# Performance work log

Measured on AMD Instinct MI355X. Metric: run time of the kernel, lower is better.

## Reference

```python
import jax, jax.numpy as jnp
import numpy as np

L, K, H = 8192, 30, 128
SCALE = 30.0
LN_EPS = 1e-5


def _ln(x, g, b):
    mu = jnp.mean(x, axis=-1, keepdims=True)
    var = jnp.mean((x - mu) ** 2, axis=-1, keepdims=True)
    return (x - mu) * jax.lax.rsqrt(var + LN_EPS) * g + b


def _gelu(x):
    return jax.nn.gelu(x, approximate=False)  # torch.nn.GELU default (exact)


def setup_inputs() -> dict:
    key = jax.random.key(0)
    ks = jax.random.split(key, 16)

    def lin(k, din, dout):
        k1, k2 = jax.random.split(k)
        w = jax.random.normal(k1, (din, dout), jnp.float32) / np.sqrt(din).astype(np.float32)
        b = jax.random.normal(k2, (dout,), jnp.float32) * 0.01
        return w, b

    inp = {}
    inp['h_V'] = jax.random.normal(ks[0], (L, H), jnp.float32)
    inp['h_E'] = jax.random.normal(ks[1], (L, K, H), jnp.float32)
    inp['E_idx'] = jax.random.randint(ks[2], (L, K), 0, L, jnp.int32)
    inp['mask_V'] = jnp.ones((L,), jnp.float32)
    inp['mask_attend'] = jnp.ones((L, K), jnp.float32)

    D_in = 3 * H  # num_hidden + num_in = 128 + 256
    inp['W1'], inp['b1'] = lin(ks[3], D_in, H)
    inp['W2'], inp['b2'] = lin(ks[4], H, H)
    inp['W3'], inp['b3'] = lin(ks[5], H, H)
    inp['W11'], inp['b11'] = lin(ks[6], D_in, H)
    inp['W12'], inp['b12'] = lin(ks[7], H, H)
    inp['W13'], inp['b13'] = lin(ks[8], H, H)
    inp['Wi'], inp['bi'] = lin(ks[9], H, 4 * H)   # PositionWiseFeedForward.W_in
    inp['Wo'], inp['bo'] = lin(ks[10], 4 * H, H)  # PositionWiseFeedForward.W_out
    inp['g1'] = jnp.ones((H,), jnp.float32); inp['be1'] = jnp.zeros((H,), jnp.float32)
    inp['g2'] = jnp.ones((H,), jnp.float32); inp['be2'] = jnp.zeros((H,), jnp.float32)
    inp['g3'] = jnp.ones((H,), jnp.float32); inp['be3'] = jnp.zeros((H,), jnp.float32)
    return inp


def _forward(h_V, h_E, E_idx, mask_V, mask_attend,
             W1, b1, W2, b2, W3, b3, W11, b11, W12, b12, W13, b13,
             Wi, bi, Wo, bo, g1, be1, g2, be2, g3, be3):
    # --- node update: gather neighbors, concat, 3-layer MLP message, masked sum ---
    h_nb = h_V[E_idx]                                   # [L,K,H] gather_nodes
    h_EV = jnp.concatenate(
        [jnp.broadcast_to(h_V[:, None, :], (L, K, H)), h_E, h_nb], axis=-1)  # [L,K,3H]
    m = _gelu(h_EV @ W1 + b1)
    m = _gelu(m @ W2 + b2)
    m = m @ W3 + b3                                     # [L,K,H]
    m = mask_attend[..., None] * m
    dh = jnp.sum(m, axis=-2) / SCALE                    # [L,H]
    h_V = _ln(h_V + dh, g1, be1)
    # --- position-wise FFN ---
    dh = _gelu(h_V @ Wi + bi) @ Wo + bo
    h_V = _ln(h_V + dh, g2, be2)
    h_V = mask_V[:, None] * h_V
    # --- edge update ---
    h_nb = h_V[E_idx]
    h_EV = jnp.concatenate(
        [jnp.broadcast_to(h_V[:, None, :], (L, K, H)), h_E, h_nb], axis=-1)
    m = _gelu(h_EV @ W11 + b11)
    m = _gelu(m @ W12 + b12)
    m = m @ W13 + b13
    h_E = _ln(h_E + m, g3, be3)
    return h_V, h_E


def reference(h_V, h_E, E_idx, mask_V, mask_attend,
              W1, b1, W2, b2, W3, b3, W11, b11, W12, b12, W13, b13,
              Wi, bi, Wo, bo, g1, be1, g2, be2, g3, be3):
    return _forward(h_V, h_E, E_idx, mask_V, mask_attend,
                    W1, b1, W2, b2, W3, b3, W11, b11, W12, b12, W13, b13,
                    Wi, bi, Wo, bo, g1, be1, g2, be2, g3, be3)
```

## Files before the change

kernel.cpp:

```cpp
#include <hip/hip_runtime.h>
#include <math.h>

typedef unsigned short u16;
typedef __bf16 bf16x8 __attribute__((ext_vector_type(8)));
typedef float f32x4 __attribute__((ext_vector_type(4)));
typedef u16 u16x8 __attribute__((ext_vector_type(8)));

#define LTOT 8192
#define KNB  30
#define HDIM 128

__device__ __forceinline__ float bf2f(u16 u){
  unsigned x = ((unsigned)u) << 16;
  return __builtin_bit_cast(float, x);
}
__device__ __forceinline__ u16 f2bf(float f){
  unsigned x = __builtin_bit_cast(unsigned, f);
  x = x + 0x7fffu + ((x >> 16) & 1u);
  return (u16)(x >> 16);
}
__device__ __forceinline__ float gelu_f(float x){
  float u = 0.7978845608028654f * (x + 0.044715f * x * x * x);
  float e = __expf(2.f * u);
  float t = 1.f - 2.f / (e + 1.f);
  return 0.5f * x * (1.f + t);
}
__device__ __forceinline__ void pack8(u16* dst, const float* s){
  float4 a = *(const float4*)s, b = *(const float4*)(s + 4);
  u16x8 p;
  p[0]=f2bf(a.x); p[1]=f2bf(a.y); p[2]=f2bf(a.z); p[3]=f2bf(a.w);
  p[4]=f2bf(b.x); p[5]=f2bf(b.y); p[6]=f2bf(b.z); p[7]=f2bf(b.w);
  *(u16x8*)dst = p;
}

struct TEnt { const float* src; u16* dst; int K; int N; int nb; };
struct TTab { TEnt e[12]; };

__global__ __launch_bounds__(256) void transpose_kernel(TTab t){
  int b = (int)blockIdx.x;
  for (int i = 0; i < 12; ++i){
    int nb = t.e[i].nb;
    if (b < nb){
      int N = t.e[i].N, Kd = t.e[i].K;
      int idx = b * 256 + (int)threadIdx.x;
      if (idx < Kd * N){
        int k = idx / N;
        int n = idx - k * N;
        t.e[i].dst[n * Kd + k] = f2bf(t.e[i].src[(long)k * N + n]);
      }
      return;
    }
    b -= nb;
  }
}

template<bool XF32>
__global__ __launch_bounds__(256) void pre_gemm_kernel(
  const void* __restrict__ X,
  const u16* __restrict__ WTa, const float* __restrict__ ba, u16* __restrict__ outa,
  const u16* __restrict__ WTc, u16* __restrict__ outc)
{
  __shared__ __align__(16) char smem[8704];
  u16* Xs = (u16*)smem;
  const int tid = threadIdx.x;
  const int wave = tid >> 6, lane = tid & 63, q = lane >> 4, s = lane & 15;
  const int row0 = (int)blockIdx.x * 32;

  for (int i = tid; i < 32 * 16; i += 256){
    int r = i >> 4, cb = i & 15;
    if (XF32) pack8(&Xs[r * 136 + cb * 8], &((const float*)X)[(long)(row0 + r) * HDIM + cb * 8]);
    else *(u16x8*)&Xs[r * 136 + cb * 8] = *(const u16x8*)&((const u16*)X)[(long)(row0 + r) * HDIM + cb * 8];
  }
  __syncthreads();
  for (int w = 0; w < 2; ++w){
    const u16* W = w ? WTc : WTa;
    u16* out = w ? outc : outa;
    f32x4 acc[2][2];
#pragma unroll
    for (int mt = 0; mt < 2; ++mt)
#pragma unroll
      for (int nt = 0; nt < 2; ++nt){ f32x4 z = {0.f,0.f,0.f,0.f}; acc[mt][nt] = z; }
    for (int kt = 0; kt < 4; ++kt){
      bf16x8 b0 = *(const bf16x8*)&W[(wave * 32 + s) * 128 + kt * 32 + q * 8];
      bf16x8 b1 = *(const bf16x8*)&W[(wave * 32 + 16 + s) * 128 + kt * 32 + q * 8];
#pragma unroll
      for (int mt = 0; mt < 2; ++mt){
        bf16x8 af = *(const bf16x8*)&Xs[(mt * 16 + s) * 136 + kt * 32 + q * 8];
        acc[mt][0] = __builtin_amdgcn_mfma_f32_16x16x32_bf16(af, b0, acc[mt][0], 0, 0, 0);
        acc[mt][1] = __builtin_amdgcn_mfma_f32_16x16x32_bf16(af, b1, acc[mt][1], 0, 0, 0);
      }
    }
#pragma unroll
    for (int nt = 0; nt < 2; ++nt){
      int col = wave * 32 + nt * 16 + s;
      float bv = w ? 0.f : ba[col];
#pragma unroll
      for (int mt = 0; mt < 2; ++mt)
#pragma unroll
        for (int r = 0; r < 4; ++r){
          int row = row0 + mt * 16 + q * 4 + r;
          out[(long)row * HDIM + col] = f2bf(acc[mt][nt][r] + bv);
        }
    }
  }
}

template<bool EDGE>
__global__ __launch_bounds__(256, 4) void msg_kernel(
  const float* __restrict__ hVin,
  const float* __restrict__ hE,
  const int* __restrict__ Eidx,
  const float* __restrict__ maskA,
  const u16* __restrict__ vsum,
  const u16* __restrict__ vcg,
  const u16* __restrict__ WTb, const u16* __restrict__ WT2, const u16* __restrict__ WT3,
  const float* __restrict__ b2, const float* __restrict__ b3,
  const float* __restrict__ gam, const float* __restrict__ bet,
  float* __restrict__ out_f32,
  u16* __restrict__ out_b16,
  float* __restrict__ outE)
{
  __shared__ __align__(16) char smem[18944];
  u16*   As   = (u16*)smem;
  float* ovl  = (float*)smem;
  float* vbuf = (float*)(smem + 17408);
  float* mbuf = (float*)(smem + 18432);
  int*   nbr  = (int*)(smem + 18688);

  const int tid = threadIdx.x;
  const int wave = tid >> 6, lane = tid & 63, q = lane >> 4, s = lane & 15;
  const int node0 = (int)blockIdx.x * 2;

  for (int i = tid; i < 64 * 16; i += 256){
    int r = i >> 4, cb = i & 15, nd = r >> 5, k = r & 31;
    if (k < KNB)
      pack8(&As[r * 136 + cb * 8], &hE[(((long)(node0 + nd) * KNB) + k) * HDIM + cb * 8]);
    else { u16x8 z = {0,0,0,0,0,0,0,0}; *(u16x8*)&As[r * 136 + cb * 8] = z; }
  }
  if (tid < 64){
    int nd = tid >> 5, k = tid & 31;
    int e = (node0 + nd) * KNB + k;
    bool v = (k < KNB);
    nbr[tid] = v ? Eidx[e] : 0;
    if (!EDGE) mbuf[tid] = v ? maskA[e] : 0.f;
  }
  vbuf[tid] = bf2f(vsum[(long)(node0 + (tid >> 7)) * HDIM + (tid & 127)]);

  f32x4 acc[4][2];
  for (int layer = 0; layer < 3; ++layer){
    const u16* W = (layer == 0) ? WTb : ((layer == 1) ? WT2 : WT3);
    __syncthreads();
#pragma unroll
    for (int mt = 0; mt < 4; ++mt){ f32x4 z = {0.f,0.f,0.f,0.f}; acc[mt][0] = z; acc[mt][1] = z; }
    for (int kt = 0; kt < 4; ++kt){
      bf16x8 b0 = *(const bf16x8*)&W[(wave * 32 + s) * 128 + kt * 32 + q * 8];
      bf16x8 b1 = *(const bf16x8*)&W[(wave * 32 + 16 + s) * 128 + kt * 32 + q * 8];
#pragma unroll
      for (int mt = 0; mt < 4; ++mt){
        bf16x8 af = *(const bf16x8*)&As[(mt * 16 + s) * 136 + kt * 32 + q * 8];
        acc[mt][0] = __builtin_amdgcn_mfma_f32_16x16x32_bf16(af, b0, acc[mt][0], 0, 0, 0);
        acc[mt][1] = __builtin_amdgcn_mfma_f32_16x16x32_bf16(af, b1, acc[mt][1], 0, 0, 0);
      }
    }
    if (layer < 2){
      __syncthreads();
#pragma unroll
      for (int nt = 0; nt < 2; ++nt){
        int col = wave * 32 + nt * 16 + s;
        float bv = (layer == 1) ? b2[col] : 0.f;
#pragma unroll
        for (int mt = 0; mt < 4; ++mt)
#pragma unroll
          for (int r = 0; r < 4; ++r){
            int row = mt * 16 + q * 4 + r;
            float v = acc[mt][nt][r] + bv;
            if (layer == 0)
              v += vbuf[((row >> 5) << 7) + col] + bf2f(vcg[(long)nbr[row] * HDIM + col]);
            As[row * 136 + col] = f2bf(gelu_f(v));
          }
      }
    }
  }
  __syncthreads();

  if (!EDGE){
    float* dh = ovl;
#pragma unroll
    for (int nt = 0; nt < 2; ++nt){
      int col = wave * 32 + nt * 16 + s;
      float b3v = b3[col];
#pragma unroll
      for (int ni = 0; ni < 2; ++ni){
        float ss = 0.f;
#pragma unroll
        for (int mh = 0; mh < 2; ++mh){
          int mt = ni * 2 + mh;
#pragma unroll
          for (int r = 0; r < 4; ++r){
            int row = mt * 16 + q * 4 + r;
            ss += (acc[mt][nt][r] + b3v) * mbuf[row];
          }
        }
        ss += __shfl_xor(ss, 16);
        ss += __shfl_xor(ss, 32);
        if (q == 0) dh[ni * 128 + col] = ss * (1.f / 30.f);
      }
    }
    __syncthreads();
    if (wave < 2){
      int node = node0 + wave;
      float x0 = hVin[(long)node * HDIM + lane]      + dh[wave * 128 + lane];
      float x1 = hVin[(long)node * HDIM + 64 + lane] + dh[wave * 128 + 64 + lane];
      float sm = x0 + x1, s2 = x0 * x0 + x1 * x1;
#pragma unroll
      for (int o = 32; o; o >>= 1){ sm += __shfl_xor(sm, o); s2 += __shfl_xor(s2, o); }
      float mu = sm * (1.f / 128.f);
      float var = fmaxf(s2 * (1.f / 128.f) - mu * mu, 0.f);
      float rs = rsqrtf(var + 1e-5f);
      float y0 = (x0 - mu) * rs * gam[lane]      + bet[lane];
      float y1 = (x1 - mu) * rs * gam[64 + lane] + bet[64 + lane];
      out_f32[(long)node * HDIM + lane]      = y0;
      out_f32[(long)node * HDIM + 64 + lane] = y1;
      out_b16[(long)node * HDIM + lane]      = f2bf(y0);
      out_b16[(long)node * HDIM + 64 + lane] = f2bf(y1);
    }
  } else {
    float* part  = ovl;
    float* part2 = ovl + 256;
    float* muv   = ovl + 512;
    float* rsv   = ovl + 576;
#pragma unroll
    for (int nt = 0; nt < 2; ++nt){
      int col = wave * 32 + nt * 16 + s;
      float b3v = b3[col];
#pragma unroll
      for (int mt = 0; mt < 4; ++mt)
#pragma unroll
        for (int r = 0; r < 4; ++r){
          int row = mt * 16 + q * 4 + r, nd = row >> 5, k = row & 31;
          float z = acc[mt][nt][r] + b3v;
          if (k < KNB) z += hE[(((long)(node0 + nd) * KNB) + k) * HDIM + col];
          acc[mt][nt][r] = z;
        }
    }
#pragma unroll
    for (int mt = 0; mt < 4; ++mt)
#pragma unroll
      for (int r = 0; r < 4; ++r){
        int row = mt * 16 + q * 4 + r;
        float ps = acc[mt][0][r] + acc[mt][1][r];
        float pq = acc[mt][0][r] * acc[mt][0][r] + acc[mt][1][r] * acc[mt][1][r];
#pragma unroll
        for (int o = 1; o < 16; o <<= 1){ ps += __shfl_xor(ps, o); pq += __shfl_xor(pq, o); }
        if (s == 0){ part[row * 4 + wave] = ps; part2[row * 4 + wave] = pq; }
      }
    __syncthreads();
    if (tid < 64){
      float sm = part[tid*4] + part[tid*4+1] + part[tid*4+2] + part[tid*4+3];
      float sq = part2[tid*4] + part2[tid*4+1] + part2[tid*4+2] + part2[tid*4+3];
      float mu = sm * (1.f / 128.f);
      float var = fmaxf(sq * (1.f / 128.f) - mu * mu, 0.f);
      muv[tid] = mu;
      rsv[tid] = rsqrtf(var + 1e-5f);
    }
    __syncthreads();
#pragma unroll
    for (int nt = 0; nt < 2; ++nt){
      int col = wave * 32 + nt * 16 + s;
      float gv = gam[col], bv = bet[col];
#pragma unroll
      for (int mt = 0; mt < 4; ++mt)
#pragma unroll
        for (int r = 0; r < 4; ++r){
          int row = mt * 16 + q * 4 + r, nd = row >> 5, k = row & 31;
          if (k < KNB){
            float y = (acc[mt][nt][r] - muv[row]) * rsv[row] * gv + bv;
            outE[(((long)(node0 + nd) * KNB) + k) * HDIM + col] = y;
          }
        }
    }
  }
}

__global__ __launch_bounds__(256) void ffn_kernel(
  const u16* __restrict__ xb, const float* __restrict__ xf,
  const u16* __restrict__ WiT,
  const u16* __restrict__ WoT,
  const float* __restrict__ bi, const float* __restrict__ bo,
  const float* __restrict__ g2, const float* __restrict__ be2,
  const float* __restrict__ maskV,
  float* __restrict__ outV, u16* __restrict__ hv2)
{
  __shared__ __align__(16) char smem[18816];
  u16*   Xs = (u16*)smem;
  u16*   Ts = (u16*)(smem + 8704);
  float* part  = (float*)(smem + 17408);
  float* part2 = part + 128;
  float* muv   = part + 256;
  float* rsv   = part + 288;
  const int tid = threadIdx.x;
  const int wave = tid >> 6, lane = tid & 63, q = lane >> 4, s = lane & 15;
  const int row0 = (int)blockIdx.x * 32;

  for (int i = tid; i < 32 * 16; i += 256){
    int r = i >> 4, cb = i & 15;
    *(u16x8*)&Xs[r * 136 + cb * 8] = *(const u16x8*)&xb[(long)(row0 + r) * HDIM + cb * 8];
  }
  f32x4 yac[2][2];
#pragma unroll
  for (int mt = 0; mt < 2; ++mt)
#pragma unroll
    for (int nt = 0; nt < 2; ++nt){ f32x4 z = {0.f,0.f,0.f,0.f}; yac[mt][nt] = z; }

  for (int j = 0; j < 4; ++j){
    __syncthreads();
    f32x4 tac[2][2];
#pragma unroll
    for (int mt = 0; mt < 2; ++mt)
#pragma unroll
      for (int nt = 0; nt < 2; ++nt){ f32x4 z = {0.f,0.f,0.f,0.f}; tac[mt][nt] = z; }
    for (int kt = 0; kt < 4; ++kt){
      bf16x8 b0 = *(const bf16x8*)&WiT[((long)(j * 128 + wave * 32 + s)) * 128 + kt * 32 + q * 8];
      bf16x8 b1 = *(const bf16x8*)&WiT[((long)(j * 128 + wave * 32 + 16 + s)) * 128 + kt * 32 + q * 8];
#pragma unroll
      for (int mt = 0; mt < 2; ++mt){
        bf16x8 af = *(const bf16x8*)&Xs[(mt * 16 + s) * 136 + kt * 32 + q * 8];
        tac[mt][0] = __builtin_amdgcn_mfma_f32_16x16x32_bf16(af, b0, tac[mt][0], 0, 0, 0);
        tac[mt][1] = __builtin_amdgcn_mfma_f32_16x16x32_bf16(af, b1, tac[mt][1], 0, 0, 0);
      }
    }
#pragma unroll
    for (int nt = 0; nt < 2; ++nt){
      int col = wave * 32 + nt * 16 + s;
      float bv = bi[j * 128 + col];
#pragma unroll
      for (int mt = 0; mt < 2; ++mt)
#pragma unroll
        for (int r = 0; r < 4; ++r){
          int row = mt * 16 + q * 4 + r;
          Ts[row * 136 + col] = f2bf(gelu_f(tac[mt][nt][r] + bv));
        }
    }
    __syncthreads();
    for (int kt = 0; kt < 4; ++kt){
      bf16x8 b0 = *(const bf16x8*)&WoT[((long)(wave * 32 + s)) * 512 + j * 128 + kt * 32 + q * 8];
      bf16x8 b1 = *(const bf16x8*)&WoT[((long)(wave * 32 + 16 + s)) * 512 + j * 128 + kt * 32 + q * 8];
#pragma unroll
      for (int mt = 0; mt < 2; ++mt){
        bf16x8 af = *(const bf16x8*)&Ts[(mt * 16 + s) * 136 + kt * 32 + q * 8];
        yac[mt][0] = __builtin_amdgcn_mfma_f32_16x16x32_bf16(af, b0, yac[mt][0], 0, 0, 0);
        yac[mt][1] = __builtin_amdgcn_mfma_f32_16x16x32_bf16(af, b1, yac[mt][1], 0, 0, 0);
      }
    }
  }
#pragma unroll
  for (int nt = 0; nt < 2; ++nt){
    int col = wave * 32 + nt * 16 + s;
    float bv = bo[col];
#pragma unroll
    for (int mt = 0; mt < 2; ++mt)
#pragma unroll
      for (int r = 0; r < 4; ++r){
        int row = mt * 16 + q * 4 + r;
        yac[mt][nt][r] += bv + xf[(long)(row0 + row) * HDIM + col];
      }
  }
#pragma unroll
  for (int mt = 0; mt < 2; ++mt)
#pragma unroll
    for (int r = 0; r < 4; ++r){
      int row = mt * 16 + q * 4 + r;
      float ps = yac[mt][0][r] + yac[mt][1][r];
      float pq = yac[mt][0][r] * yac[mt][0][r] + yac[mt][1][r] * yac[mt][1][r];
#pragma unroll
      for (int o = 1; o < 16; o <<= 1){ ps += __shfl_xor(ps, o); pq += __shfl_xor(pq, o); }
      if (s == 0){ part[row * 4 + wave] = ps; part2[row * 4 + wave] = pq; }
    }
  __syncthreads();
  if (tid < 32){
    float sm = part[tid*4] + part[tid*4+1] + part[tid*4+2] + part[tid*4+3];
    float sq = part2[tid*4] + part2[tid*4+1] + part2[tid*4+2] + part2[tid*4+3];
    float mu = sm * (1.f / 128.f);
    float var = fmaxf(sq * (1.f / 128.f) - mu * mu, 0.f);
    muv[tid] = mu;
    rsv[tid] = rsqrtf(var + 1e-5f);
  }
  __syncthreads();
#pragma unroll
  for (int nt = 0; nt < 2; ++nt){
    int col = wave * 32 + nt * 16 + s;
    float gv = g2[col], bv = be2[col];
#pragma unroll
    for (int mt = 0; mt < 2; ++mt)
#pragma unroll
      for (int r = 0; r < 4; ++r){
        int row = mt * 16 + q * 4 + r;
        float y = (yac[mt][nt][r] - muv[row]) * rsv[row] * gv + bv;
        y *= maskV[row0 + row];
        outV[(long)(row0 + row) * HDIM + col] = y;
        hv2[(long)(row0 + row) * HDIM + col] = f2bf(y);
      }
  }
}

extern "C" void kernel_launch(void* const* d_in, const int* in_sizes, int n_in,
                              void* d_out, int out_size, void* d_ws, size_t ws_size,
                              hipStream_t stream) {
  const float* hV    = (const float*)d_in[0];
  const float* hE    = (const float*)d_in[1];
  const int*   Eidx  = (const int*)d_in[2];
  const float* maskV = (const float*)d_in[3];
  const float* maskA = (const float*)d_in[4];
  const float* W1  = (const float*)d_in[5];  const float* b1  = (const float*)d_in[6];
  const float* W2  = (const float*)d_in[7];  const float* b2  = (const float*)d_in[8];
  const float* W3  = (const float*)d_in[9];  const float* b3  = (const float*)d_in[10];
  const float* W11 = (const float*)d_in[11]; const float* b11 = (const float*)d_in[12];
  const float* W12 = (const float*)d_in[13]; const float* b12 = (const float*)d_in[14];
  const float* W13 = (const float*)d_in[15]; const float* b13 = (const float*)d_in[16];
  const float* Wi  = (const float*)d_in[17]; const float* bi  = (const float*)d_in[18];
  const float* Wo  = (const float*)d_in[19]; const float* bo  = (const float*)d_in[20];
  const float* g1  = (const float*)d_in[21]; const float* be1 = (const float*)d_in[22];
  const float* g2  = (const float*)d_in[23]; const float* be2 = (const float*)d_in[24];
  const float* g3  = (const float*)d_in[25]; const float* be3 = (const float*)d_in[26];

  char* ws = (char*)d_ws;
  u16* wt = (u16*)ws;
  u16* wtW1a  = wt;
  u16* wtW1b  = wt + 16384;
  u16* wtW1c  = wt + 32768;
  u16* wtW2   = wt + 49152;
  u16* wtW3   = wt + 65536;
  u16* wtW11a = wt + 81920;
  u16* wtW11b = wt + 98304;
  u16* wtW11c = wt + 114688;
  u16* wtW12  = wt + 131072;
  u16* wtW13  = wt + 147456;
  u16* wtWi   = wt + 163840;
  u16* wtWo   = wt + 229376;
  size_t off = 589824;
  u16* vsum1   = (u16*)(ws + off); off += 2097152;
  u16* vc      = (u16*)(ws + off); off += 2097152;
  u16* vsum11  = (u16*)(ws + off); off += 2097152;
  u16* vc2     = (u16*)(ws + off); off += 2097152;
  float* hv1_f32 = (float*)(ws + off); off += 4194304;
  u16*   hv1_b16 = (u16*)(ws + off);   off += 2097152;
  u16*   hv2_b16 = (u16*)(ws + off);   off += 2097152;

  float* outV = (float*)d_out;
  float* outE = (float*)d_out + (long)LTOT * HDIM;

  TTab tt;
  tt.e[0]  = { W1,          wtW1a,  128, 128, 64 };
  tt.e[1]  = { W1 + 16384,  wtW1b,  128, 128, 64 };
  tt.e[2]  = { W1 + 32768,  wtW1c,  128, 128, 64 };
  tt.e[3]  = { W2,          wtW2,   128, 128, 64 };
  tt.e[4]  = { W3,          wtW3,   128, 128, 64 };
  tt.e[5]  = { W11,         wtW11a, 128, 128, 64 };
  tt.e[6]  = { W11 + 16384, wtW11b, 128, 128, 64 };
  tt.e[7]  = { W11 + 32768, wtW11c, 128, 128, 64 };
  tt.e[8]  = { W12,         wtW12,  128, 128, 64 };
  tt.e[9]  = { W13,         wtW13,  128, 128, 64 };
  tt.e[10] = { Wi,          wtWi,   128, 512, 256 };
  tt.e[11] = { Wo,          wtWo,   512, 128, 256 };
  transpose_kernel<<<dim3(1152), dim3(256), 0, stream>>>(tt);

  pre_gemm_kernel<true><<<dim3(256), dim3(256), 0, stream>>>(
      hV, wtW1a, b1, vsum1, wtW1c, vc);
  msg_kernel<false><<<dim3(4096), dim3(256), 0, stream>>>(
      hV, hE, Eidx, maskA, vsum1, vc, wtW1b, wtW2, wtW3, b2, b3, g1, be1,
      hv1_f32, hv1_b16, nullptr);
  ffn_kernel<<<dim3(256), dim3(256), 0, stream>>>(
      hv1_b16, hv1_f32, wtWi, wtWo, bi, bo, g2, be2, maskV, outV, hv2_b16);
  pre_gemm_kernel<false><<<dim3(256), dim3(256), 0, stream>>>(
      hv2_b16, wtW11a, b11, vsum11, wtW11c, vc2);
  msg_kernel<true><<<dim3(4096), dim3(256), 0, stream>>>(
      hV, hE, Eidx, maskA, vsum11, vc2, wtW11b, wtW12, wtW13, b12, b13, g3, be3,
      hv1_f32, hv1_b16, outE);
}
```

Before: 463.2 us.

## Stage gathered neighbor rows in LDS and cheapen GELU and bf16 conversion

The kernel now copies the gathered neighbor rows (vcg indexed by nbr) into a new LDS buffer with coalesced 16-byte loads before the first MFMA layer. The layer-0 epilogue then reads those values from LDS instead of issuing scattered 2-byte global loads, and the per-node vbuf values are hoisted into registers. GELU uses an exp2 form with a hardware reciprocal, and bf16 conversion uses the native cast. LDS use roughly doubles, which may lower occupancy, and the tanh-approximation GELU becomes slightly less accurate.

Measured after the change: 442.5 us. 1.05x faster.

```diff
diff --git a/kernel.cpp b/kernel.cpp
--- a/kernel.cpp
+++ b/kernel.cpp
@@ -15,15 +15,22 @@
   return __builtin_bit_cast(float, x);
 }
 __device__ __forceinline__ u16 f2bf(float f){
-  unsigned x = __builtin_bit_cast(unsigned, f);
-  x = x + 0x7fffu + ((x >> 16) & 1u);
-  return (u16)(x >> 16);
+  __bf16 h = (__bf16)f;
+  return __builtin_bit_cast(u16, h);
+}
+__device__ __forceinline__ float fast_exp2(float x){
+#if __has_builtin(__builtin_amdgcn_exp2f)
+  return __builtin_amdgcn_exp2f(x);
+#else
+  return exp2f(x);
+#endif
 }
 __device__ __forceinline__ float gelu_f(float x){
-  float u = 0.7978845608028654f * (x + 0.044715f * x * x * x);
-  float e = __expf(2.f * u);
-  float t = 1.f - 2.f / (e + 1.f);
-  return 0.5f * x * (1.f + t);
+  float x2 = x * x;
+  float g  = x * (2.3022082f + 0.10294324f * x2);
+  float e  = fast_exp2(g);
+  float r  = __builtin_amdgcn_rcpf(e + 1.f);
+  return x * (1.f - r);
 }
 __device__ __forceinline__ void pack8(u16* dst, const float* s){
   float4 a = *(const float4*)s, b = *(const float4*)(s + 4);
@@ -120,12 +127,13 @@
   u16* __restrict__ out_b16,
   float* __restrict__ outE)
 {
-  __shared__ __align__(16) char smem[18944];
+  __shared__ __align__(16) char smem[36352];
   u16*   As   = (u16*)smem;
   float* ovl  = (float*)smem;
-  float* vbuf = (float*)(smem + 17408);
-  float* mbuf = (float*)(smem + 18432);
-  int*   nbr  = (int*)(smem + 18688);
+  u16*   Vs   = (u16*)(smem + 17408);
+  float* vbuf = (float*)(smem + 34816);
+  float* mbuf = (float*)(smem + 35840);
+  int*   nbr  = (int*)(smem + 36096);
 
   const int tid = threadIdx.x;
   const int wave = tid >> 6, lane = tid & 63, q = lane >> 4, s = lane & 15;
@@ -146,10 +154,17 @@
   }
   vbuf[tid] = bf2f(vsum[(long)(node0 + (tid >> 7)) * HDIM + (tid & 127)]);
 
+  __syncthreads();
+
+  for (int i = tid; i < 64 * 16; i += 256){
+    int r = i >> 4, cb = i & 15;
+    *(u16x8*)&Vs[r * 136 + cb * 8] = *(const u16x8*)&vcg[(long)nbr[r] * HDIM + cb * 8];
+  }
+
   f32x4 acc[4][2];
   for (int layer = 0; layer < 3; ++layer){
     const u16* W = (layer == 0) ? WTb : ((layer == 1) ? WT2 : WT3);
-    __syncthreads();
+    if (layer) __syncthreads();
 #pragma unroll
     for (int mt = 0; mt < 4; ++mt){ f32x4 z = {0.f,0.f,0.f,0.f}; acc[mt][0] = z; acc[mt][1] = z; }
     for (int kt = 0; kt < 4; ++kt){
@@ -168,6 +183,8 @@
       for (int nt = 0; nt < 2; ++nt){
         int col = wave * 32 + nt * 16 + s;
         float bv = (layer == 1) ? b2[col] : 0.f;
+        float vb0 = 0.f, vb1 = 0.f;
+        if (layer == 0){ vb0 = vbuf[col]; vb1 = vbuf[128 + col]; }
 #pragma unroll
         for (int mt = 0; mt < 4; ++mt)
 #pragma unroll
@@ -175,7 +192,7 @@
             int row = mt * 16 + q * 4 + r;
             float v = acc[mt][nt][r] + bv;
             if (layer == 0)
-              v += vbuf[((row >> 5) << 7) + col] + bf2f(vcg[(long)nbr[row] * HDIM + col]);
+              v += (mt < 2 ? vb0 : vb1) + bf2f(Vs[row * 136 + col]);
             As[row * 136 + col] = f2bf(gelu_f(v));
           }
       }
```
